# Kernel optimization log

Measured on AMD Instinct MI355X. Metric: run time of the kernel, lower is better.

The kernel has to match this reference:

```python
import jax, jax.numpy as jnp
import numpy as np

B, S, D = 2, 2048, 1024
E, N, HID = 8, 4, 4096

def setup_inputs() -> dict:
    key = jax.random.key(0)
    ks = jax.random.split(key, 6)
    x = jax.random.normal(ks[0], (B, S, D), dtype=jnp.float32)
    w_router = jax.random.normal(ks[1], (E, D), dtype=jnp.float32) * 0.02
    A_fc = jax.random.normal(ks[2], (E, N, N, N), dtype=jnp.float32) * 0.5
    S_fc = jax.random.normal(ks[3], (E, N, HID // N, D // N), dtype=jnp.float32) * (1.0 / np.sqrt(D))
    A_proj = jax.random.normal(ks[4], (E, N, N, N), dtype=jnp.float32) * 0.5
    S_proj = jax.random.normal(ks[5], (E, N, D // N, HID // N), dtype=jnp.float32) * (1.0 / np.sqrt(HID))
    return {"x": x, "w_router": w_router, "A_fc": A_fc, "S_fc": S_fc, "A_proj": A_proj, "S_proj": S_proj}

def _phm(Xn, A, S):
    # Xn: [T, n, s_in], S: [n, s_out, s_in], A: [n, n, n] -> [T, n, s_out]
    T_ = jnp.einsum('bkl,iol->bkio', Xn, S)
    return jnp.einsum('ijk,bkio->bjo', A, T_)

def reference(x, w_router, A_fc, S_fc, A_proj, S_proj):
    e_num, n = A_fc.shape[0], A_fc.shape[1]
    d = x.shape[-1]
    flat = x.reshape(-1, d)                      # [T, D]
    T = flat.shape[0]
    logits = flat @ w_router.T                   # [T, E]
    probs = jax.nn.softmax(logits, axis=-1)
    expert_idx = jnp.argmax(logits, axis=-1)     # [T]
    tpe = jnp.zeros((e_num,), flat.dtype).at[expert_idx].add(1.0)
    frac = tpe / T
    aux_loss = jnp.sum(frac * probs.mean(axis=0)) * e_num
    Xn = flat.reshape(T, n, d // n)
    out = jnp.zeros_like(flat)
    for e in range(e_num):                        # small fixed expert loop
        h = _phm(Xn, A_fc[e], S_fc[e]).reshape(T, -1)   # [T, HID]
        h = jnp.where(h >= 0, h, 0.5 * h)               # leaky_relu slope 0.5
        Hn = (h * h).reshape(T, n, -1)
        y = _phm(Hn, A_proj[e], S_proj[e]).reshape(T, d)
        out = out + jnp.where((expert_idx == e)[:, None], y, jnp.zeros((), flat.dtype))
    return out.reshape(x.shape), aux_loss
```

## Files before the change

kernel.cpp:

```cpp
#include <hip/hip_runtime.h>
#include <hip/hip_bf16.h>


#define T_TOK 4096
#define DIM   1024
#define NEXP  8
#define HIDD  4096
#define SLOTS 5120

static constexpr size_t OFF_WFC   = 0;
static constexpr size_t OFF_WPROJ = 67108864ull;
static constexpr size_t OFF_XB    = 134217728ull;
static constexpr size_t OFF_H     = 144703488ull;
static constexpr size_t OFF_BSUM  = 186646528ull;
static constexpr size_t OFF_EIDX  = OFF_BSUM + 1024*8*8;
static constexpr size_t OFF_TOK   = OFF_EIDX + (size_t)T_TOK*4;
static constexpr size_t OFF_CNT   = OFF_TOK + (size_t)SLOTS*4;

typedef __attribute__((ext_vector_type(8))) short short8;
typedef __attribute__((ext_vector_type(4))) float f32x4;

static __device__ __forceinline__ ushort f2bf(float f) {
    __hip_bfloat16 h = __float2bfloat16(f);
    return __builtin_bit_cast(ushort, h);
}

static __device__ __forceinline__ float bf2f(ushort u) {
    return __builtin_bit_cast(float, (unsigned)u << 16);
}

static __device__ __forceinline__ ushort4 f4bf(float4 v) {
    ushort4 b;
    b.x = f2bf(v.x); b.y = f2bf(v.y); b.z = f2bf(v.z); b.w = f2bf(v.w);
    return b;
}

static __device__ __forceinline__ void gload_lds16(const ushort* g, ushort* l) {
    __builtin_amdgcn_global_load_lds((const __attribute__((address_space(1))) void*)g,
                                     (__attribute__((address_space(3))) void*)l,
                                     16, 0, 0);
}

__global__ __launch_bounds__(256) void front_k(const float* __restrict__ x,
                                               const float* __restrict__ wr,
                                               double* __restrict__ bsum,
                                               int* __restrict__ eidx,
                                               ushort* __restrict__ xb)
{
    __shared__ double shp[4][8];
    int tid = threadIdx.x;
    int w = tid >> 6, lane = tid & 63;
    int t = blockIdx.x * 4 + w;
    const float4* xr = (const float4*)(x + (size_t)t * DIM);
    float4 xv[4];
#pragma unroll
    for (int q = 0; q < 4; q++) xv[q] = xr[q * 64 + lane];
    ushort4* xo = (ushort4*)(xb + (size_t)t * DIM);
#pragma unroll
    for (int q = 0; q < 4; q++) xo[q * 64 + lane] = f4bf(xv[q]);
    double lg[8];
#pragma unroll
    for (int e = 0; e < 8; e++) {
        const float4* wv = (const float4*)(wr + (size_t)e * DIM);
        double s = 0.0;
#pragma unroll
        for (int q = 0; q < 4; q++) {
            float4 a = xv[q], b = wv[q * 64 + lane];
            s += (double)a.x * b.x + (double)a.y * b.y + (double)a.z * b.z + (double)a.w * b.w;
        }
#pragma unroll
        for (int d = 1; d < 64; d <<= 1) s += __shfl_xor(s, d);
        lg[e] = s;
    }
    double m = lg[0];
#pragma unroll
    for (int e = 1; e < 8; e++) m = lg[e] > m ? lg[e] : m;
    double ex[8], sum = 0.0;
#pragma unroll
    for (int e = 0; e < 8; e++) { ex[e] = exp(lg[e] - m); sum += ex[e]; }
    if (lane < 8) shp[w][lane] = ex[lane] / sum;
    if (lane == 0) {
        int am = 0; double bv = lg[0];
#pragma unroll
        for (int e = 1; e < 8; e++) if (lg[e] > bv) { bv = lg[e]; am = e; }
        eidx[t] = am;
    }
    __syncthreads();
    if (tid < 8)
        bsum[(size_t)blockIdx.x * 8 + tid] =
            shp[0][tid] + shp[1][tid] + shp[2][tid] + shp[3][tid];
}

__global__ __launch_bounds__(256) void plan_k(const double* __restrict__ bsum,
                                              const int* __restrict__ eidx,
                                              int* __restrict__ counts,
                                              int* __restrict__ offsets,
                                              int* __restrict__ tok,
                                              float* __restrict__ auxout,
                                              const float* __restrict__ Afc,
                                              const float* __restrict__ Sfc,
                                              ushort* __restrict__ Wfc)
{
    __shared__ int hist[256][8];
    __shared__ double red[256][8];
    __shared__ int offs[8];
    __shared__ float Ash[64];
    int tid = threadIdx.x;
    if (blockIdx.x > 0) {
        int b2 = blockIdx.x - 1;
        int e = b2 >> 10, o = b2 & 1023;
        if (tid < 64) Ash[tid] = Afc[e * 64 + tid];
        __syncthreads();
        int k = tid >> 6, lq = tid & 63;
        float4 sv[4];
#pragma unroll
        for (int i = 0; i < 4; i++)
            sv[i] = *(const float4*)&Sfc[((size_t)(e * 4 + i) * 1024 + o) * 256 + lq * 4];
        size_t base = (size_t)e * 4194304ull;
#pragma unroll
        for (int j = 0; j < 4; j++) {
            float a0 = Ash[j * 4 + k], a1 = Ash[16 + j * 4 + k];
            float a2 = Ash[32 + j * 4 + k], a3 = Ash[48 + j * 4 + k];
            float4 v;
            v.x = a0 * sv[0].x + a1 * sv[1].x + a2 * sv[2].x + a3 * sv[3].x;
            v.y = a0 * sv[0].y + a1 * sv[1].y + a2 * sv[2].y + a3 * sv[3].y;
            v.z = a0 * sv[0].z + a1 * sv[1].z + a2 * sv[2].z + a3 * sv[3].z;
            v.w = a0 * sv[0].w + a1 * sv[1].w + a2 * sv[2].w + a3 * sv[3].w;
            *(ushort4*)&Wfc[base + (size_t)(j * 1024 + o) * 1024 + k * 256 + lq * 4] = f4bf(v);
        }
        return;
    }
    for (int i = tid; i < SLOTS; i += 256) tok[i] = -1;
    int base = tid * 16;
    int le[16];
    int lc[8] = {0,0,0,0,0,0,0,0};
#pragma unroll
    for (int j = 0; j < 16; j++) { le[j] = eidx[base + j]; lc[le[j]]++; }
#pragma unroll
    for (int e = 0; e < 8; e++) hist[tid][e] = lc[e];
    __syncthreads();
    for (int s = 1; s < 256; s <<= 1) {
        int v[8];
        if (tid >= s) {
#pragma unroll
            for (int e = 0; e < 8; e++) v[e] = hist[tid - s][e];
        }
        __syncthreads();
        if (tid >= s) {
#pragma unroll
            for (int e = 0; e < 8; e++) hist[tid][e] += v[e];
        }
        __syncthreads();
    }
    int myBase[8];
#pragma unroll
    for (int e = 0; e < 8; e++) myBase[e] = hist[tid][e] - lc[e];
    if (tid == 0) {
        int off = 0;
#pragma unroll
        for (int e = 0; e < 8; e++) {
            int c = hist[255][e];
            counts[e] = c;
            offsets[e] = off; offs[e] = off;
            off += (c + 127) & ~127;
        }
    }
    __syncthreads();
    int cur[8];
#pragma unroll
    for (int e = 0; e < 8; e++) cur[e] = myBase[e];
#pragma unroll
    for (int j = 0; j < 16; j++) {
        int e = le[j];
        tok[offs[e] + cur[e]++] = base + j;
    }
    double ps[8] = {0, 0, 0, 0, 0, 0, 0, 0};
    for (int b = tid; b < 1024; b += 256) {
#pragma unroll
        for (int e = 0; e < 8; e++) ps[e] += bsum[(size_t)b * 8 + e];
    }
#pragma unroll
    for (int e = 0; e < 8; e++) red[tid][e] = ps[e];
    __syncthreads();
    for (int s = 128; s > 0; s >>= 1) {
        if (tid < s) {
#pragma unroll
            for (int e = 0; e < 8; e++) red[tid][e] += red[tid + s][e];
        }
        __syncthreads();
    }
    if (tid == 0) {
        double aux = 0.0;
#pragma unroll
        for (int e = 0; e < 8; e++)
            aux += ((double)hist[255][e] / T_TOK) * (red[0][e] / T_TOK);
        auxout[0] = (float)(aux * NEXP);
    }
}

__global__ __launch_bounds__(256, 2) void mid_k(const ushort* __restrict__ xb,
                                                const ushort* __restrict__ Wfc,
                                                ushort* __restrict__ h,
                                                const int* __restrict__ counts,
                                                const int* __restrict__ offsets,
                                                const int* __restrict__ tok,
                                                const float* __restrict__ Apj,
                                                const float* __restrict__ Spj,
                                                ushort* __restrict__ Wpj)
{
    __shared__ __align__(16) ushort As[128 * 64];
    __shared__ __align__(16) ushort Bs[256 * 64];
    __shared__ float Ashf[64];
    int b = blockIdx.x;
    int tid = threadIdx.x;
    if (b >= 640) {
        int b2 = b - 640;
        int e = b2 >> 8, o = b2 & 255;
        if (tid < 64) Ashf[tid] = Apj[e * 64 + tid];
        __syncthreads();
        float4 sv[4];
#pragma unroll
        for (int i = 0; i < 4; i++)
            sv[i] = *(const float4*)&Spj[((size_t)(e * 4 + i) * 256 + o) * 1024 + tid * 4];
        size_t base = (size_t)e * 4194304ull;
#pragma unroll
        for (int j = 0; j < 4; j++)
#pragma unroll
            for (int k = 0; k < 4; k++) {
                float a0 = Ashf[j * 4 + k], a1 = Ashf[16 + j * 4 + k];
                float a2 = Ashf[32 + j * 4 + k], a3 = Ashf[48 + j * 4 + k];
                float4 v;
                v.x = a0 * sv[0].x + a1 * sv[1].x + a2 * sv[2].x + a3 * sv[3].x;
                v.y = a0 * sv[0].y + a1 * sv[1].y + a2 * sv[2].y + a3 * sv[3].y;
                v.z = a0 * sv[0].z + a1 * sv[1].z + a2 * sv[2].z + a3 * sv[3].z;
                v.w = a0 * sv[0].w + a1 * sv[1].w + a2 * sv[2].w + a3 * sv[3].w;
                *(ushort4*)&Wpj[base + (size_t)(j * 256 + o) * 4096 + k * 1024 + tid * 4] = f4bf(v);
            }
        return;
    }
    constexpr int KDIM = 1024;
    constexpr int NDIM = 4096;
    int r = b >> 3;
    int nb = (b & 7) * 2 + r / 40;
    int ms = r % 40;
    int e = -1, mt = 0, acct = 0;
#pragma unroll
    for (int i = 0; i < 8; i++) {
        int tiles = (counts[i] + 127) >> 7;
        if (e < 0 && ms < acct + tiles) { e = i; mt = ms - acct; }
        acct += tiles;
    }
    if (e < 0) return;
    int m_base = offsets[e] + mt * 128;
    int n_base = nb * 256;
    int w = tid >> 6, lane = tid & 63;
    int wm = w >> 1, wn = w & 1;
    const ushort* Bb = Wfc + (size_t)e * NDIM * KDIM + (size_t)n_base * KDIM;
    int lr = lane >> 3;
    int lcs = (((lane & 7) ^ lr) << 3);
    const ushort* arow[4];
#pragma unroll
    for (int i = 0; i < 4; i++) {
        int sl = m_base + i * 32 + w * 8 + lr;
        int rt = tok[sl]; if (rt < 0) rt = 0;
        arow[i] = xb + (size_t)rt * KDIM + lcs;
    }
    f32x4 acc[4][8];
#pragma unroll
    for (int i = 0; i < 4; i++)
#pragma unroll
        for (int j = 0; j < 8; j++) acc[i][j] = (f32x4){0.f, 0.f, 0.f, 0.f};

    for (int t = 0; t < KDIM / 64; t++) {
        int k0 = t * 64;
#pragma unroll
        for (int i = 0; i < 4; i++)
            gload_lds16(arow[i] + k0, &As[(i * 32 + w * 8) * 64]);
#pragma unroll
        for (int i = 0; i < 8; i++) {
            int r0 = i * 32 + w * 8;
            gload_lds16(Bb + (size_t)(r0 + lr) * KDIM + k0 + lcs, &Bs[r0 * 64]);
        }
        __syncthreads();
#pragma unroll
        for (int ks = 0; ks < 2; ks++) {
            short8 a[4], bfr[8];
            int ca = (((ks * 4 + (lane >> 4)) ^ (lane & 7)) << 3);
#pragma unroll
            for (int f = 0; f < 4; f++)
                a[f] = *(const short8*)&As[(wm * 64 + f * 16 + (lane & 15)) * 64 + ca];
#pragma unroll
            for (int f = 0; f < 8; f++)
                bfr[f] = *(const short8*)&Bs[(wn * 128 + f * 16 + (lane & 15)) * 64 + ca];
#pragma unroll
            for (int mf = 0; mf < 4; mf++)
#pragma unroll
                for (int nf = 0; nf < 8; nf++)
                    acc[mf][nf] = __builtin_amdgcn_mfma_f32_16x16x32_bf16(a[mf], bfr[nf], acc[mf][nf], 0, 0, 0);
        }
        __syncthreads();
    }

    int col0 = n_base + wn * 128;
    int row0 = wm * 64 + (lane >> 4) * 4;
#pragma unroll
    for (int mf = 0; mf < 4; mf++)
#pragma unroll
        for (int nf = 0; nf < 8; nf++) {
            int col = col0 + nf * 16 + (lane & 15);
#pragma unroll
            for (int rg = 0; rg < 4; rg++) {
                float v = acc[mf][nf][rg];
                v = v >= 0.f ? v : 0.5f * v;
                v = v * v;
                h[(size_t)(m_base + row0 + mf * 16 + rg) * NDIM + col] = f2bf(v);
            }
        }
}

__global__ __launch_bounds__(256, 2) void proj_k(const ushort* __restrict__ h,
                                                 const ushort* __restrict__ Wpj,
                                                 ushort* __restrict__ Part,
                                                 const int* __restrict__ counts,
                                                 const int* __restrict__ offsets)
{
    __shared__ __align__(16) ushort As[128 * 64];
    __shared__ __align__(16) ushort Bs[256 * 64];
    constexpr int KDIM = 4096;
    constexpr int NDIM = 1024;
    constexpr int KSUB = 2048;
    int b = blockIdx.x;
    int nb = (b & 7) >> 1;
    int split = b & 1;
    int ms = b >> 3;
    int e = -1, mt = 0, acct = 0;
#pragma unroll
    for (int i = 0; i < 8; i++) {
        int tiles = (counts[i] + 127) >> 7;
        if (e < 0 && ms < acct + tiles) { e = i; mt = ms - acct; }
        acct += tiles;
    }
    if (e < 0) return;
    int m_base = offsets[e] + mt * 128;
    int n_base = nb * 256;
    int tid = threadIdx.x, w = tid >> 6, lane = tid & 63;
    int wm = w >> 1, wn = w & 1;
    int lr = lane >> 3;
    int lcs = (((lane & 7) ^ lr) << 3);
    int kbase = split * KSUB;
    const ushort* Bb = Wpj + (size_t)e * NDIM * KDIM + (size_t)n_base * KDIM + kbase;
    const ushort* arow[4];
#pragma unroll
    for (int i = 0; i < 4; i++)
        arow[i] = h + (size_t)(m_base + i * 32 + w * 8 + lr) * KDIM + kbase + lcs;
    f32x4 acc[4][8];
#pragma unroll
    for (int i = 0; i < 4; i++)
#pragma unroll
        for (int j = 0; j < 8; j++) acc[i][j] = (f32x4){0.f, 0.f, 0.f, 0.f};

    for (int t = 0; t < KSUB / 64; t++) {
        int k0 = t * 64;
#pragma unroll
        for (int i = 0; i < 4; i++)
            gload_lds16(arow[i] + k0, &As[(i * 32 + w * 8) * 64]);
#pragma unroll
        for (int i = 0; i < 8; i++) {
            int r0 = i * 32 + w * 8;
            gload_lds16(Bb + (size_t)(r0 + lr) * KDIM + k0 + lcs, &Bs[r0 * 64]);
        }
        __syncthreads();
#pragma unroll
        for (int ks = 0; ks < 2; ks++) {
            short8 a[4], bfr[8];
            int ca = (((ks * 4 + (lane >> 4)) ^ (lane & 7)) << 3);
#pragma unroll
            for (int f = 0; f < 4; f++)
                a[f] = *(const short8*)&As[(wm * 64 + f * 16 + (lane & 15)) * 64 + ca];
#pragma unroll
            for (int f = 0; f < 8; f++)
                bfr[f] = *(const short8*)&Bs[(wn * 128 + f * 16 + (lane & 15)) * 64 + ca];
#pragma unroll
            for (int mf = 0; mf < 4; mf++)
#pragma unroll
                for (int nf = 0; nf < 8; nf++)
                    acc[mf][nf] = __builtin_amdgcn_mfma_f32_16x16x32_bf16(a[mf], bfr[nf], acc[mf][nf], 0, 0, 0);
        }
        __syncthreads();
    }

    ushort* P = Part + (size_t)split * SLOTS * NDIM;
    int col0 = n_base + wn * 128;
    int row0 = wm * 64 + (lane >> 4) * 4;
#pragma unroll
    for (int mf = 0; mf < 4; mf++)
#pragma unroll
        for (int nf = 0; nf < 8; nf++) {
            int col = col0 + nf * 16 + (lane & 15);
#pragma unroll
            for (int rg = 0; rg < 4; rg++)
                P[(size_t)(m_base + row0 + mf * 16 + rg) * NDIM + col] = f2bf(acc[mf][nf][rg]);
        }
}

__global__ __launch_bounds__(256) void reduce_k(const ushort* __restrict__ P,
                                                const int* __restrict__ tok,
                                                float* __restrict__ out)
{
    int slot = blockIdx.x;
    int t = tok[slot];
    if (t < 0) return;
    int i = threadIdx.x;
    const ushort4* p0 = (const ushort4*)(P + (size_t)slot * DIM);
    const ushort4* p1 = (const ushort4*)(P + (size_t)(SLOTS + slot) * DIM);
    ushort4 a = p0[i], b = p1[i];
    float4* o = (float4*)(out + (size_t)t * DIM);
    o[i] = (float4){bf2f(a.x) + bf2f(b.x), bf2f(a.y) + bf2f(b.y),
                    bf2f(a.z) + bf2f(b.z), bf2f(a.w) + bf2f(b.w)};
}

extern "C" void kernel_launch(void* const* d_in, const int* in_sizes, int n_in,
                              void* d_out, int out_size, void* d_ws, size_t ws_size,
                              hipStream_t stream)
{
    const float* x    = (const float*)d_in[0];
    const float* wr   = (const float*)d_in[1];
    const float* A_fc = (const float*)d_in[2];
    const float* S_fc = (const float*)d_in[3];
    const float* A_pj = (const float*)d_in[4];
    const float* S_pj = (const float*)d_in[5];
    float* out = (float*)d_out;
    char* ws = (char*)d_ws;

    ushort* Wfc   = (ushort*)(ws + OFF_WFC);
    ushort* Part  = (ushort*)(ws + OFF_WFC);
    ushort* Wpj   = (ushort*)(ws + OFF_WPROJ);
    ushort* xb    = (ushort*)(ws + OFF_XB);
    ushort* h     = (ushort*)(ws + OFF_H);
    double* bsum  = (double*)(ws + OFF_BSUM);
    int*    eidx  = (int*)(ws + OFF_EIDX);
    int*    tok   = (int*)(ws + OFF_TOK);
    int*    counts  = (int*)(ws + OFF_CNT);
    int*    offsets = counts + 16;

    front_k<<<T_TOK / 4, 256, 0, stream>>>(x, wr, bsum, eidx, xb);
    plan_k<<<1 + 8192, 256, 0, stream>>>(bsum, eidx, counts, offsets, tok,
                                         out + (size_t)T_TOK * DIM,
                                         A_fc, S_fc, Wfc);
    mid_k<<<640 + 2048, 256, 0, stream>>>(xb, Wfc, h, counts, offsets, tok,
                                          A_pj, S_pj, Wpj);
    proj_k<<<320, 256, 0, stream>>>(h, Wpj, Part, counts, offsets);
    reduce_k<<<SLOTS, 256, 0, stream>>>(Part, tok, out);
}
```

Baseline: 167.5 us.

## Fuse router and plan kernels via last-block atomic, grid-stride reduce

```diff
diff --git a/kernel.cpp b/kernel.cpp
--- a/kernel.cpp
+++ b/kernel.cpp
@@ -45,69 +45,25 @@
                                                const float* __restrict__ wr,
                                                double* __restrict__ bsum,
                                                int* __restrict__ eidx,
-                                               ushort* __restrict__ xb)
+                                               ushort* __restrict__ xb,
+                                               const float* __restrict__ Afc,
+                                               const float* __restrict__ Sfc,
+                                               ushort* __restrict__ Wfc,
+                                               int* __restrict__ counts,
+                                               int* __restrict__ offsets,
+                                               int* __restrict__ tok,
+                                               float* __restrict__ auxout,
+                                               int* __restrict__ done)
 {
     __shared__ double shp[4][8];
-    int tid = threadIdx.x;
-    int w = tid >> 6, lane = tid & 63;
-    int t = blockIdx.x * 4 + w;
-    const float4* xr = (const float4*)(x + (size_t)t * DIM);
-    float4 xv[4];
-#pragma unroll
-    for (int q = 0; q < 4; q++) xv[q] = xr[q * 64 + lane];
-    ushort4* xo = (ushort4*)(xb + (size_t)t * DIM);
-#pragma unroll
-    for (int q = 0; q < 4; q++) xo[q * 64 + lane] = f4bf(xv[q]);
-    double lg[8];
-#pragma unroll
-    for (int e = 0; e < 8; e++) {
-        const float4* wv = (const float4*)(wr + (size_t)e * DIM);
-        double s = 0.0;
-#pragma unroll
-        for (int q = 0; q < 4; q++) {
-            float4 a = xv[q], b = wv[q * 64 + lane];
-            s += (double)a.x * b.x + (double)a.y * b.y + (double)a.z * b.z + (double)a.w * b.w;
-        }
-#pragma unroll
-        for (int d = 1; d < 64; d <<= 1) s += __shfl_xor(s, d);
-        lg[e] = s;
-    }
-    double m = lg[0];
-#pragma unroll
-    for (int e = 1; e < 8; e++) m = lg[e] > m ? lg[e] : m;
-    double ex[8], sum = 0.0;
-#pragma unroll
-    for (int e = 0; e < 8; e++) { ex[e] = exp(lg[e] - m); sum += ex[e]; }
-    if (lane < 8) shp[w][lane] = ex[lane] / sum;
-    if (lane == 0) {
-        int am = 0; double bv = lg[0];
-#pragma unroll
-        for (int e = 1; e < 8; e++) if (lg[e] > bv) { bv = lg[e]; am = e; }
-        eidx[t] = am;
-    }
-    __syncthreads();
-    if (tid < 8)
-        bsum[(size_t)blockIdx.x * 8 + tid] =
-            shp[0][tid] + shp[1][tid] + shp[2][tid] + shp[3][tid];
-}
-
-__global__ __launch_bounds__(256) void plan_k(const double* __restrict__ bsum,
-                                              const int* __restrict__ eidx,
-                                              int* __restrict__ counts,
-                                              int* __restrict__ offsets,
-                                              int* __restrict__ tok,
-                                              float* __restrict__ auxout,
-                                              const float* __restrict__ Afc,
-                                              const float* __restrict__ Sfc,
-                                              ushort* __restrict__ Wfc)
-{
+    __shared__ float Ash[64];
     __shared__ int hist[256][8];
     __shared__ double red[256][8];
     __shared__ int offs[8];
-    __shared__ float Ash[64];
+    __shared__ int winner;
     int tid = threadIdx.x;
-    if (blockIdx.x > 0) {
-        int b2 = blockIdx.x - 1;
+    if (blockIdx.x >= 1024) {
+        int b2 = blockIdx.x - 1024;
         int e = b2 >> 10, o = b2 & 1023;
         if (tid < 64) Ash[tid] = Afc[e * 64 + tid];
         __syncthreads();
@@ -130,6 +86,57 @@
         }
         return;
     }
+    {
+        int w = tid >> 6, lane = tid & 63;
+        int t = blockIdx.x * 4 + w;
+        const float4* xr = (const float4*)(x + (size_t)t * DIM);
+        float4 xv[4];
+#pragma unroll
+        for (int q = 0; q < 4; q++) xv[q] = xr[q * 64 + lane];
+        ushort4* xo = (ushort4*)(xb + (size_t)t * DIM);
+#pragma unroll
+        for (int q = 0; q < 4; q++) xo[q * 64 + lane] = f4bf(xv[q]);
+        double lg[8];
+#pragma unroll
+        for (int e = 0; e < 8; e++) {
+            const float4* wv = (const float4*)(wr + (size_t)e * DIM);
+            double s = 0.0;
+#pragma unroll
+            for (int q = 0; q < 4; q++) {
+                float4 a = xv[q], b = wv[q * 64 + lane];
+                s += (double)a.x * b.x + (double)a.y * b.y + (double)a.z * b.z + (double)a.w * b.w;
+            }
+#pragma unroll
+            for (int d = 1; d < 64; d <<= 1) s += __shfl_xor(s, d);
+            lg[e] = s;
+        }
+        float lf[8];
+#pragma unroll
+        for (int e = 0; e < 8; e++) lf[e] = (float)lg[e];
+        float mf = lf[0];
+#pragma unroll
+        for (int e = 1; e < 8; e++) mf = fmaxf(mf, lf[e]);
+        float ex[8], sum = 0.f;
+#pragma unroll
+        for (int e = 0; e < 8; e++) { ex[e] = __expf(lf[e] - mf); sum += ex[e]; }
+        if (lane < 8) shp[w][lane] = (double)(ex[lane] / sum);
+        if (lane == 0) {
+            int am = 0; double bv = lg[0];
+#pragma unroll
+            for (int e = 1; e < 8; e++) if (lg[e] > bv) { bv = lg[e]; am = e; }
+            eidx[t] = am;
+        }
+        __syncthreads();
+        if (tid < 8)
+            bsum[(size_t)blockIdx.x * 8 + tid] =
+                shp[0][tid] + shp[1][tid] + shp[2][tid] + shp[3][tid];
+    }
+    __syncthreads();
+    __threadfence();
+    if (tid == 0) winner = (atomicAdd(done, 1) == 1023) ? 1 : 0;
+    __syncthreads();
+    if (!winner) return;
+    __threadfence();
     for (int i = tid; i < SLOTS; i += 256) tok[i] = -1;
     int base = tid * 16;
     int le[16];
@@ -407,16 +414,17 @@
                                                 const int* __restrict__ tok,
                                                 float* __restrict__ out)
 {
-    int slot = blockIdx.x;
-    int t = tok[slot];
-    if (t < 0) return;
-    int i = threadIdx.x;
-    const ushort4* p0 = (const ushort4*)(P + (size_t)slot * DIM);
-    const ushort4* p1 = (const ushort4*)(P + (size_t)(SLOTS + slot) * DIM);
-    ushort4 a = p0[i], b = p1[i];
-    float4* o = (float4*)(out + (size_t)t * DIM);
-    o[i] = (float4){bf2f(a.x) + bf2f(b.x), bf2f(a.y) + bf2f(b.y),
-                    bf2f(a.z) + bf2f(b.z), bf2f(a.w) + bf2f(b.w)};
+    for (int slot = blockIdx.x; slot < SLOTS; slot += gridDim.x) {
+        int t = tok[slot];
+        if (t < 0) continue;
+        int i = threadIdx.x;
+        const ushort4* p0 = (const ushort4*)(P + (size_t)slot * DIM);
+        const ushort4* p1 = (const ushort4*)(P + (size_t)(SLOTS + slot) * DIM);
+        ushort4 a = p0[i], b = p1[i];
+        float4* o = (float4*)(out + (size_t)t * DIM);
+        o[i] = (float4){bf2f(a.x) + bf2f(b.x), bf2f(a.y) + bf2f(b.y),
+                        bf2f(a.z) + bf2f(b.z), bf2f(a.w) + bf2f(b.w)};
+    }
 }
 
 extern "C" void kernel_launch(void* const* d_in, const int* in_sizes, int n_in,
@@ -442,13 +450,15 @@
     int*    tok   = (int*)(ws + OFF_TOK);
     int*    counts  = (int*)(ws + OFF_CNT);
     int*    offsets = counts + 16;
-
-    front_k<<<T_TOK / 4, 256, 0, stream>>>(x, wr, bsum, eidx, xb);
-    plan_k<<<1 + 8192, 256, 0, stream>>>(bsum, eidx, counts, offsets, tok,
-                                         out + (size_t)T_TOK * DIM,
-                                         A_fc, S_fc, Wfc);
+    int*    done    = counts + 32;
+
+    hipMemsetAsync(done, 0, 4, stream);
+    front_k<<<1024 + 8192, 256, 0, stream>>>(x, wr, bsum, eidx, xb,
+                                             A_fc, S_fc, Wfc,
+                                             counts, offsets, tok,
+                                             out + (size_t)T_TOK * DIM, done);
     mid_k<<<640 + 2048, 256, 0, stream>>>(xb, Wfc, h, counts, offsets, tok,
                                           A_pj, S_pj, Wpj);
     proj_k<<<320, 256, 0, stream>>>(h, Wpj, Part, counts, offsets);
-    reduce_k<<<SLOTS, 256, 0, stream>>>(Part, tok, out);
-}
+    reduce_k<<<1280, 256, 0, stream>>>(Part, tok, out);
+}
```

Result: slower. 277.0 us (+65.4%).
